# Kernel tuning notes

Measured on AMD Instinct MI355X. Metric: run time of the kernel, lower is better.

## Reference

```python
import jax, jax.numpy as jnp
import numpy as np

N = 100000      # nodes
E = 1250000     # edges
D = 64          # hidden_units == dim_node_features
DE = 7          # edge feature dim (OGBG-PPA)
L = 5           # num_layers
G = 128         # graphs in batch
T = 37          # classes


def setup_inputs() -> dict:
    key = jax.random.key(0)
    ks = jax.random.split(key, 12)
    x = jax.random.normal(ks[0], (N, D), dtype=jnp.float32)
    edge_index = jax.random.randint(ks[1], (2, E), 0, N, dtype=jnp.int64)
    edge_attr = jax.random.uniform(ks[2], (E, DE), dtype=jnp.float32)
    batch = jnp.sort(jax.random.randint(ks[3], (N,), 0, G, dtype=jnp.int64))
    s_e = 1.0 / np.sqrt(DE)
    s_d = 1.0 / np.sqrt(D)
    s_p = 1.0 / np.sqrt(L * D)
    W_edge = jax.random.normal(ks[4], (DE, D), dtype=jnp.float32) * s_e  # shared edge encoder
    b_edge = jnp.zeros((D,), jnp.float32)
    W_mlp = jax.random.normal(ks[5], (L, D, D), dtype=jnp.float32) * s_d  # per-layer MLP
    b_mlp = jnp.zeros((L, D), jnp.float32)
    eps = jnp.zeros((L,), jnp.float32)  # torch.Tensor([0]) per layer
    W_pred = jax.random.normal(ks[6], (L * D, T), dtype=jnp.float32) * s_p
    b_pred = jnp.zeros((T,), jnp.float32)
    return {"x": x, "edge_index": edge_index, "edge_attr": edge_attr, "batch": batch,
            "W_edge": W_edge, "b_edge": b_edge, "eps": eps,
            "W_mlp": W_mlp, "b_mlp": b_mlp, "W_pred": W_pred, "b_pred": b_pred}


def reference(x, edge_index, edge_attr, batch, W_edge, b_edge, eps, W_mlp, b_mlp, W_pred, b_pred):
    src, dst = edge_index[0], edge_index[1]  # PyG source_to_target: x_j = x[src], aggregate at dst
    # shared edge encoder -> identical output every layer; compute once
    edge_emb = edge_attr @ W_edge + b_edge  # [E, D]
    h = x
    outs = []
    for i in range(L):
        msg = jax.nn.relu(h[src] + edge_emb)                      # gather + fuse  [E, D]
        agg = jax.ops.segment_sum(msg, dst, num_segments=N)       # scatter-add    [N, D]
        h = jax.nn.relu(((1.0 + eps[i]) * h + agg) @ W_mlp[i] + b_mlp[i])
        outs.append(h)
    node_emb = jnp.concatenate(outs, axis=1)                      # [N, L*D]
    # predictor: per-graph mean pool + linear readout
    g_sum = jax.ops.segment_sum(node_emb, batch, num_segments=G)  # [G, L*D]
    cnt = jax.ops.segment_sum(jnp.ones((N, 1), node_emb.dtype), batch, num_segments=G)
    g = g_sum / jnp.maximum(cnt, 1.0)
    return g @ W_pred + b_pred                                    # [G, T]
```

## Files before the change

kernel.cpp:

```cpp
#include <hip/hip_runtime.h>
#include <hip/hip_bf16.h>

#define DD   64
#define NL   5
#define NT   37
#define LD   (NL*DD)
#define PB   16
#define NBMAX 512

typedef __attribute__((ext_vector_type(8))) short short8;
typedef __attribute__((ext_vector_type(4))) float f32x4;
typedef __attribute__((ext_vector_type(4))) int   i32x4;
typedef __attribute__((ext_vector_type(2))) int   i32x2;

static __device__ __forceinline__ int padq(int d) { return (d + PB - 1) & ~(PB - 1); }
static __device__ __forceinline__ short bf16_bits(float f) {
    __hip_bfloat16 h = __float2bfloat16(f);
    return __builtin_bit_cast(short, h);
}
static __device__ __forceinline__ float bf2f(short s) {
    return __int_as_float(((int)(unsigned short)s) << 16);
}

__global__ void init_kernel(const float* __restrict__ x, __hip_bfloat16* __restrict__ hb,
                            size_t n1, const float* __restrict__ W,
                            __hip_bfloat16* __restrict__ Wt, int n2,
                            const float* __restrict__ W_edge, const float* __restrict__ b_edge,
                            __hip_bfloat16* __restrict__ webt, int* __restrict__ bcnt,
                            const int* __restrict__ dst, int* __restrict__ deg, int E,
                            int do_deg) {
    size_t i = (size_t)blockIdx.x * blockDim.x + threadIdx.x;
    if (i < n1) {
        hb[i] = __float2bfloat16(x[i]);
    } else if (i < n1 + (size_t)n2) {
        size_t id = i - n1;
        int l = (int)(id / (DD * DD));
        int r = (int)(id % (DD * DD));
        int c = r / DD, k = r % DD;
        Wt[(size_t)l * DD * DD + c * DD + k] =
            __float2bfloat16(W[(size_t)l * DD * DD + k * DD + c]);
    } else if (i < n1 + (size_t)n2 + 2048) {
        int id = (int)(i - n1 - (size_t)n2);
        int f = id >> 5, k = id & 31;
        float v = (k < 7) ? W_edge[k * DD + f] : (k == 7 ? b_edge[f] : 0.f);
        webt[id] = __float2bfloat16(v);
    } else if (i < n1 + (size_t)n2 + 2048 + NBMAX) {
        bcnt[i - n1 - (size_t)n2 - 2048] = 0;
    } else if (do_deg) {
        size_t e = i - n1 - (size_t)n2 - 2048 - NBMAX;
        if (e < (size_t)E) atomicAdd(&deg[dst[e]], 1);
    }
}

__global__ void bhist_kernel(const int* __restrict__ dst, int* __restrict__ bcnt, int E) {
    __shared__ int h[NBMAX];
    int tid = threadIdx.x;
    h[tid] = 0; h[tid + 256] = 0;
    __syncthreads();
    int base = blockIdx.x * 4096;
#pragma unroll
    for (int j = 0; j < 16; ++j) {
        int e = base + j * 256 + tid;
        if (e < E) atomicAdd(&h[dst[e] >> 8], 1);
    }
    __syncthreads();
    int c0 = h[tid], c1 = h[tid + 256];
    if (c0) atomicAdd(&bcnt[tid], c0);
    if (c1) atomicAdd(&bcnt[tid + 256], c1);
}

__global__ void bscan_kernel(const int* __restrict__ bcnt, int* __restrict__ boff,
                             int* __restrict__ bcur) {
    __shared__ int sm[256];
    int tid = threadIdx.x;
    int v0 = bcnt[2 * tid], v1 = bcnt[2 * tid + 1];
    int s = v0 + v1;
    sm[tid] = s;
    __syncthreads();
    for (int off = 1; off < 256; off <<= 1) {
        int t = (tid >= off) ? sm[tid - off] : 0;
        __syncthreads();
        sm[tid] += t;
        __syncthreads();
    }
    int p = sm[tid] - s;
    boff[2 * tid] = p;     bcur[2 * tid] = p;     p += v0;
    boff[2 * tid + 1] = p; bcur[2 * tid + 1] = p; p += v1;
    if (tid == 255) boff[512] = p;
}

__global__ void pscat_kernel(const int* __restrict__ dst, int* __restrict__ bcur,
                             i32x2* __restrict__ stage, int E) {
    __shared__ int h[NBMAX];
    __shared__ int runb[NBMAX];
    int tid = threadIdx.x;
    h[tid] = 0; h[tid + 256] = 0;
    __syncthreads();
    int base = blockIdx.x * 4096;
    int d[16];
#pragma unroll
    for (int j = 0; j < 16; ++j) {
        int e = base + j * 256 + tid;
        d[j] = (e < E) ? dst[e] : -1;
        if (d[j] >= 0) atomicAdd(&h[d[j] >> 8], 1);
    }
    __syncthreads();
    int c0 = h[tid], c1 = h[tid + 256];
    runb[tid]       = c0 ? atomicAdd(&bcur[tid], c0) : 0;
    runb[tid + 256] = c1 ? atomicAdd(&bcur[tid + 256], c1) : 0;
    __syncthreads();
    h[tid] = 0; h[tid + 256] = 0;
    __syncthreads();
#pragma unroll
    for (int j = 0; j < 16; ++j) {
        if (d[j] >= 0) {
            int b = d[j] >> 8;
            int r = atomicAdd(&h[b], 1);
            i32x2 pr; pr[0] = base + j * 256 + tid; pr[1] = d[j];
            stage[runb[b] + r] = pr;
        }
    }
}

__global__ void bdeg_kernel(const i32x2* __restrict__ stage, const int* __restrict__ boff,
                            int* __restrict__ deg, int n) {
    __shared__ int cnt[256];
    int tid = threadIdx.x;
    int b = blockIdx.x;
    cnt[tid] = 0;
    __syncthreads();
    int s = boff[b], e = boff[b + 1];
    for (int j = s + tid; j < e; j += 256)
        atomicAdd(&cnt[stage[j][1] & 255], 1);
    __syncthreads();
    int node = b * 256 + tid;
    if (node < n) deg[node] = cnt[tid];
}

template<bool PACKED>
__global__ void assign_kernel(i32x2* __restrict__ stage, const int* __restrict__ boff,
                              const int* __restrict__ rowptr,
                              short* __restrict__ eab, int* __restrict__ srcv,
                              int* __restrict__ col, int n) {
    __shared__ int cur[256];
    int tid = threadIdx.x;
    int b = blockIdx.x;
    int node = b * 256 + tid;
    cur[tid] = (node < n) ? rowptr[node] : 0;
    __syncthreads();
    int s = boff[b], e = boff[b + 1];
    for (int j = s + tid; j < e; j += 256) {
        int d = stage[j][1];
        int slot = atomicAdd(&cur[d & 255], 1);
        stage[j][1] = slot;
    }
    __syncthreads();
    if (node < n) {
        int endp = rowptr[node + 1];
        for (int i = cur[tid]; i < endp; ++i) {
            srcv[i] = 0;
            if (PACKED) {
                i32x4 z = {0, 0, 0, 0};
                *((i32x4*)(eab + (size_t)i * 8)) = z;
            } else {
                col[i] = 0;
            }
        }
    }
}

template<bool PACKED>
__global__ void build_kernel(const i32x2* __restrict__ stage, const int* __restrict__ src,
                             const float* __restrict__ ea,
                             short* __restrict__ eab, int* __restrict__ srcv,
                             int* __restrict__ col, int E) {
    int j = blockIdx.x * blockDim.x + threadIdx.x;
    if (j >= E) return;
    i32x2 pr = stage[j];
    int eid = pr[0], slot = pr[1];
    srcv[slot] = src[eid];
    if (PACKED) {
        const float* a = ea + (size_t)eid * 7;
        short8 r;
#pragma unroll
        for (int k = 0; k < 7; ++k) r[k] = bf16_bits(a[k]);
        r[7] = (short)0x3F80;
        *((i32x4*)(eab + (size_t)slot * 8)) = __builtin_bit_cast(i32x4, r);
    } else {
        col[slot] = eid;
    }
}

__global__ void chunksum_kernel(const int* __restrict__ deg, int* __restrict__ csum, int n) {
    __shared__ int sm[256];
    int tid = threadIdx.x;
    int base = blockIdx.x * 1024 + tid * 4;
    int s = 0;
#pragma unroll
    for (int j = 0; j < 4; ++j) s += (base + j < n) ? padq(deg[base + j]) : 0;
    sm[tid] = s;
    __syncthreads();
    for (int off = 128; off > 0; off >>= 1) {
        if (tid < off) sm[tid] += sm[tid + off];
        __syncthreads();
    }
    if (tid == 0) csum[blockIdx.x] = sm[0];
}

__global__ void scansums_kernel(int* __restrict__ csum, int nc, int* __restrict__ tot) {
    __shared__ int sm[256];
    int tid = threadIdx.x;
    int base = tid * 4;
    int v[4]; int s = 0;
#pragma unroll
    for (int j = 0; j < 4; ++j) { v[j] = (base + j < nc) ? csum[base + j] : 0; s += v[j]; }
    sm[tid] = s;
    __syncthreads();
    for (int off = 1; off < 256; off <<= 1) {
        int t = (tid >= off) ? sm[tid - off] : 0;
        __syncthreads();
        sm[tid] += t;
        __syncthreads();
    }
    int p = sm[tid] - s;
#pragma unroll
    for (int j = 0; j < 4; ++j) { if (base + j < nc) csum[base + j] = p; p += v[j]; }
    if (tid == 255) *tot = p;
}

__global__ void chunkscan_kernel(const int* __restrict__ deg, const int* __restrict__ csum,
                                 int* __restrict__ rowptr, int* __restrict__ cursor, int n) {
    __shared__ int sm[256];
    int tid = threadIdx.x;
    int base = blockIdx.x * 1024 + tid * 4;
    int v[4]; int s = 0;
#pragma unroll
    for (int j = 0; j < 4; ++j) { v[j] = (base + j < n) ? padq(deg[base + j]) : 0; s += v[j]; }
    sm[tid] = s;
    __syncthreads();
    for (int off = 1; off < 256; off <<= 1) {
        int t = (tid >= off) ? sm[tid - off] : 0;
        __syncthreads();
        sm[tid] += t;
        __syncthreads();
    }
    int p = sm[tid] - s + csum[blockIdx.x];
#pragma unroll
    for (int j = 0; j < 4; ++j) {
        if (base + j < n) { rowptr[base + j] = p; cursor[base + j] = p; }
        p += v[j];
    }
}

__global__ void fillpos_kernel(const int* __restrict__ dst, int* __restrict__ cursor,
                               int* __restrict__ col, int E) {
    int e = blockIdx.x * blockDim.x + threadIdx.x;
    if (e >= E) return;
    int p = atomicAdd(&cursor[dst[e]], 1);
    col[p] = e;
}

__global__ void padmark_kernel(const int* __restrict__ deg, const int* __restrict__ rowptr,
                               int* __restrict__ col, int n) {
    int v = blockIdx.x * blockDim.x + threadIdx.x;
    if (v >= n) return;
    int s = rowptr[v] + deg[v];
    int e = rowptr[v + 1];
    for (int i = s; i < e; ++i) col[i] = -1;
}

template<bool PACKED>
__global__ void gfill_kernel(const int* __restrict__ col, const int* __restrict__ src,
                             const float* __restrict__ ea, const int* __restrict__ rowptrN,
                             short* __restrict__ eab, int* __restrict__ srcv,
                             int* __restrict__ colw) {
    int slot = blockIdx.x * blockDim.x + threadIdx.x;
    if (slot >= *rowptrN) return;
    int e = col[slot];
    int s = 0;
    short8 r;
#pragma unroll
    for (int k = 0; k < 8; ++k) r[k] = 0;
    if (e >= 0) {
        s = src[e];
        if (PACKED) {
            const float* a = ea + (size_t)e * 7;
#pragma unroll
            for (int k = 0; k < 7; ++k) r[k] = bf16_bits(a[k]);
            r[7] = (short)0x3F80;
        }
    } else if (!PACKED) {
        colw[slot] = 0;
    }
    __builtin_nontemporal_store(s, &srcv[slot]);
    if (PACKED) {
        i32x4 ri = __builtin_bit_cast(i32x4, r);
        __builtin_nontemporal_store(ri, (i32x4*)(eab + (size_t)slot * 8));
    }
}

template<bool PACKED>
__global__ void fill_kernel(const int* __restrict__ dst, const int* __restrict__ src,
                            const float* __restrict__ ea, int* __restrict__ cursor,
                            short* __restrict__ eab, int* __restrict__ col,
                            int* __restrict__ srcv, int E) {
    int e = blockIdx.x * blockDim.x + threadIdx.x;
    if (e >= E) return;
    int p = atomicAdd(&cursor[dst[e]], 1);
    int s = src[e];
    __builtin_nontemporal_store(s, &srcv[p]);
    if (PACKED) {
        const float* a = ea + (size_t)e * 7;
        short8 r;
#pragma unroll
        for (int k = 0; k < 7; ++k) r[k] = bf16_bits(a[k]);
        r[7] = (short)0x3F80;
        i32x4 ri = __builtin_bit_cast(i32x4, r);
        __builtin_nontemporal_store(ri, (i32x4*)(eab + (size_t)p * 8));
    } else {
        __builtin_nontemporal_store(e, &col[p]);
    }
}

__global__ void padfill_kernel(const int* __restrict__ deg, const int* __restrict__ rowptr,
                               int* __restrict__ srcv, int* __restrict__ col,
                               int has_col, int n) {
    int v = blockIdx.x * blockDim.x + threadIdx.x;
    if (v >= n) return;
    int s = rowptr[v] + deg[v];
    int e = rowptr[v + 1];
    for (int i = s; i < e; ++i) {
        srcv[i] = 0;
        if (has_col) col[i] = 0;
    }
}

template<bool PACKED>
static __device__ __forceinline__ float row_partial(
    const __hip_bfloat16* __restrict__ hb_in, const short* __restrict__ eab,
    const int* __restrict__ col, const float* __restrict__ ea,
    const int* __restrict__ srcv, int beg, int dv, int lane,
    const float* __restrict__ we, float be) {
    float acc = 0.f;
    int end = beg + dv;
    for (int p = beg; p < end; p += PB) {
        int mm = end - p;
        int S[PB];
#pragma unroll
        for (int j = 0; j < PB; ++j) S[j] = srcv[p + j];
        __hip_bfloat16 hv[PB];
#pragma unroll
        for (int j = 0; j < PB; ++j) hv[j] = hb_in[(size_t)S[j] * DD + lane];
        float ev[PB][7];
        if (PACKED) {
            short8 eb[PB];
#pragma unroll
            for (int j = 0; j < PB; ++j)
                eb[j] = *((const short8*)(eab + (size_t)(p + j) * 8));
#pragma unroll
            for (int j = 0; j < PB; ++j)
#pragma unroll
                for (int k = 0; k < 7; ++k) ev[j][k] = bf2f(eb[j][k]);
        } else {
            int EJ[PB];
#pragma unroll
            for (int j = 0; j < PB; ++j) EJ[j] = col[p + j];
#pragma unroll
            for (int j = 0; j < PB; ++j) {
                const float* a = ea + (size_t)EJ[j] * 7;
#pragma unroll
                for (int k = 0; k < 7; ++k) ev[j][k] = a[k];
            }
        }
#pragma unroll
        for (int j = 0; j < PB; ++j) {
            if (j < mm) {
                float emb = be + ev[j][0] * we[0] + ev[j][1] * we[1] + ev[j][2] * we[2]
                               + ev[j][3] * we[3] + ev[j][4] * we[4] + ev[j][5] * we[5]
                               + ev[j][6] * we[6];
                float tv = __bfloat162float(hv[j]) + emb;
                acc += (tv > 0.f) ? tv : 0.f;
            }
        }
    }
    return acc;
}

template<bool PACKED>
static __device__ __forceinline__ void agg_pair(
    const __hip_bfloat16* __restrict__ hb_in, const short* __restrict__ eab,
    const int* __restrict__ col, const float* __restrict__ ea,
    const int* __restrict__ srcv, int beg0, int d0, int beg1, int d1, bool has1,
    int lane, const float* __restrict__ we, float be, float& acc0, float& acc1) {
    acc0 = row_partial<PACKED>(hb_in, eab, col, ea, srcv, beg0, d0, lane, we, be);
    acc1 = 0.f;
    if (has1)
        acc1 = row_partial<PACKED>(hb_in, eab, col, ea, srcv, beg1, d1, lane, we, be);
}

__global__ __launch_bounds__(256, 4)
void aggmlp_kernel(const __hip_bfloat16* __restrict__ hb_in,
                   const short* __restrict__ eab, const int* __restrict__ srcv,
                   const int* __restrict__ rowptr, const int* __restrict__ deg,
                   const float* __restrict__ W_edge, const float* __restrict__ b_edge,
                   const __hip_bfloat16* __restrict__ webt,
                   const float* __restrict__ eps, int layer,
                   const __hip_bfloat16* __restrict__ Wt, const float* __restrict__ bmlp,
                   __hip_bfloat16* __restrict__ hb_out, int n) {
    __shared__ __align__(16) short uls[16][72];
    const unsigned short* hbu = (const unsigned short*)hb_in;
    int tid = threadIdx.x;
    int lane = tid & 63;
    int wv = __builtin_amdgcn_readfirstlane(tid >> 6);
    int base = blockIdx.x * 16;
    int colx = lane & 15;
    int q = lane >> 4;

    float we[7];
#pragma unroll
    for (int k = 0; k < 7; ++k) we[k] = W_edge[k * DD + lane];
    float be = b_edge[lane];
    float epsv = 1.f + eps[layer];

    short8 wb[4];
#pragma unroll
    for (int t = 0; t < 4; ++t)
        wb[t] = *((const short8*)(webt + (size_t)(t * 16 + colx) * 32 + q * 8));

#pragma unroll
    for (int nd = 0; nd < 4; ++nd) {
        int v = base + wv * 4 + nd;
        if (v < n) {
            int p = rowptr[v];
            int d = deg[v];
            float nodeacc;
            if (d >= 1 && d <= PB) {
                short8 a = {0, 0, 0, 0, 0, 0, 0, 0};
                if (q == 0)
                    a = *((const short8*)(eab + (size_t)(p + colx) * 8));
                int sr0 = srcv[p + 4 * q + 0];
                int sr1 = srcv[p + 4 * q + 1];
                int sr2 = srcv[p + 4 * q + 2];
                int sr3 = srcv[p + 4 * q + 3];
                f32x4 z = {0.f, 0.f, 0.f, 0.f};
                f32x4 emb[4];
#pragma unroll
                for (int t = 0; t < 4; ++t)
                    emb[t] = __builtin_amdgcn_mfma_f32_16x16x32_bf16(a, wb[t], z, 0, 0, 0);
                unsigned short hv[4][4];
#pragma unroll
                for (int t = 0; t < 4; ++t) {
                    hv[0][t] = hbu[(size_t)sr0 * DD + t * 16 + colx];
                    hv[1][t] = hbu[(size_t)sr1 * DD + t * 16 + colx];
                    hv[2][t] = hbu[(size_t)sr2 * DD + t * 16 + colx];
                    hv[3][t] = hbu[(size_t)sr3 * DD + t * 16 + colx];
                }
                float ts[4];
#pragma unroll
                for (int t = 0; t < 4; ++t) {
                    float s = 0.f;
#pragma unroll
                    for (int r = 0; r < 4; ++r) {
                        float tv = __int_as_float((int)hv[r][t] << 16) + emb[t][r];
                        float rv = ((4 * q + r) < d) ? ((tv > 0.f) ? tv : 0.f) : 0.f;
                        s += rv;
                    }
                    s += __shfl_xor(s, 16, 64);
                    s += __shfl_xor(s, 32, 64);
                    ts[t] = s;
                }
                nodeacc = (q == 0) ? ts[0] : (q == 1) ? ts[1] : (q == 2) ? ts[2] : ts[3];
            } else {
                nodeacc = row_partial<true>(hb_in, eab, nullptr, nullptr, srcv,
                                            p, d, lane, we, be);
            }
            float self = __int_as_float((int)hbu[(size_t)v * DD + lane] << 16);
            uls[wv * 4 + nd][lane] = bf16_bits(epsv * self + nodeacc);
        }
    }
    __syncthreads();

    if (wv == 0) {
        short8 wf[4][2];
#pragma unroll
        for (int t = 0; t < 4; ++t)
#pragma unroll
            for (int s = 0; s < 2; ++s)
                wf[t][s] = *((const short8*)(Wt + (size_t)(t * 16 + colx) * DD + s * 32 + q * 8));
        float bias[4];
#pragma unroll
        for (int t = 0; t < 4; ++t) bias[t] = bmlp[t * 16 + colx];

        short8 a0 = *((const short8*)&uls[colx][q * 8]);
        short8 a1 = *((const short8*)&uls[colx][32 + q * 8]);

        f32x4 acc[4] = {{0.f, 0.f, 0.f, 0.f}, {0.f, 0.f, 0.f, 0.f},
                        {0.f, 0.f, 0.f, 0.f}, {0.f, 0.f, 0.f, 0.f}};
#pragma unroll
        for (int t = 0; t < 4; ++t) {
            acc[t] = __builtin_amdgcn_mfma_f32_16x16x32_bf16(a0, wf[t][0], acc[t], 0, 0, 0);
            acc[t] = __builtin_amdgcn_mfma_f32_16x16x32_bf16(a1, wf[t][1], acc[t], 0, 0, 0);
        }
#pragma unroll
        for (int r = 0; r < 4; ++r) {
            int v = base + q * 4 + r;
            if (v < n) {
#pragma unroll
                for (int t = 0; t < 4; ++t) {
                    float val = acc[t][r] + bias[t];
                    val = (val > 0.f) ? val : 0.f;
                    hb_out[(size_t)v * DD + t * 16 + colx] = __float2bfloat16(val);
                }
            }
        }
    }
}

template<bool PACKED>
__global__ __launch_bounds__(256, 4)
void agg_kernel(const __hip_bfloat16* __restrict__ hb_in,
                const short* __restrict__ eab,
                const int* __restrict__ col, const int* __restrict__ srcv,
                const float* __restrict__ ea,
                const int* __restrict__ rowptr, const int* __restrict__ deg,
                const float* __restrict__ W_edge, const float* __restrict__ b_edge,
                const float* __restrict__ eps, int layer,
                __hip_bfloat16* __restrict__ u, int n) {
    int lane = threadIdx.x & 63;
    int wid = __builtin_amdgcn_readfirstlane(blockIdx.x * 4 + (threadIdx.x >> 6));
    int v0 = wid * 2;
    if (v0 >= n) return;

    float we[7];
#pragma unroll
    for (int k = 0; k < 7; ++k) we[k] = W_edge[k * DD + lane];
    float be = b_edge[lane];
    float epsv = 1.f + eps[layer];

    int beg0 = rowptr[v0];
    int d0   = deg[v0];
    bool has1 = (v0 + 1) < n;
    int beg1 = has1 ? rowptr[v0 + 1] : 0;
    int d1   = has1 ? deg[v0 + 1] : 0;

    float acc0, acc1;
    agg_pair<PACKED>(hb_in, eab, col, ea, srcv, beg0, d0, beg1, d1, has1,
                     lane, we, be, acc0, acc1);

    float self0 = __bfloat162float(hb_in[(size_t)v0 * DD + lane]);
    u[(size_t)v0 * DD + lane] = __float2bfloat16(epsv * self0 + acc0);
    if (has1) {
        float self1 = __bfloat162float(hb_in[(size_t)(v0 + 1) * DD + lane]);
        u[(size_t)(v0 + 1) * DD + lane] = __float2bfloat16(epsv * self1 + acc1);
    }
}

__global__ __launch_bounds__(256, 4)
void mlp_mfma_kernel(const __hip_bfloat16* __restrict__ u,
                     const __hip_bfloat16* __restrict__ Wt,
                     const float* __restrict__ bmlp,
                     __hip_bfloat16* __restrict__ hb_out, int n) {
    int lane = threadIdx.x & 63;
    int wid  = threadIdx.x >> 6;
    int colx = lane & 15;
    int quad = lane >> 4;
    int v0 = __builtin_amdgcn_readfirstlane((blockIdx.x * 4 + wid) * 16);
    if (v0 >= n) return;

    short8 wf[4][2];
#pragma unroll
    for (int t = 0; t < 4; ++t)
#pragma unroll
        for (int s = 0; s < 2; ++s)
            wf[t][s] = *((const short8*)(Wt + (size_t)(t * 16 + colx) * DD + s * 32 + quad * 8));
    float bias[4];
#pragma unroll
    for (int t = 0; t < 4; ++t) bias[t] = bmlp[t * 16 + colx];

    int vr = v0 + colx;
    int vrc = (vr < n) ? vr : (n - 1);
    const __hip_bfloat16* up = u + (size_t)vrc * DD;
    short8 a0 = *((const short8*)(up + quad * 8));
    short8 a1 = *((const short8*)(up + 32 + quad * 8));

    f32x4 acc[4] = {{0.f, 0.f, 0.f, 0.f}, {0.f, 0.f, 0.f, 0.f},
                    {0.f, 0.f, 0.f, 0.f}, {0.f, 0.f, 0.f, 0.f}};
#pragma unroll
    for (int t = 0; t < 4; ++t) {
        acc[t] = __builtin_amdgcn_mfma_f32_16x16x32_bf16(a0, wf[t][0], acc[t], 0, 0, 0);
        acc[t] = __builtin_amdgcn_mfma_f32_16x16x32_bf16(a1, wf[t][1], acc[t], 0, 0, 0);
    }

#pragma unroll
    for (int r = 0; r < 4; ++r) {
        int v = v0 + quad * 4 + r;
        if (v < n) {
#pragma unroll
            for (int t = 0; t < 4; ++t) {
                float val = acc[t][r] + bias[t];
                val = (val > 0.f) ? val : 0.f;
                hb_out[(size_t)v * DD + t * 16 + colx] = __float2bfloat16(val);
            }
        }
    }
}

__global__ void pool_part_kernel(const __hip_bfloat16* __restrict__ htabs, size_t lstride,
                                 const int* __restrict__ batch,
                                 float* __restrict__ g_sum, int n, int G) {
    __shared__ float part[4][DD];
    __shared__ int bnd[2];
    int g = blockIdx.x / NL;
    int q = blockIdx.x % NL;
    int tid = threadIdx.x;
    if (tid < 2) {
        int target = g + tid;
        int lo = 0, hi = n;
        while (lo < hi) { int mid = (lo + hi) >> 1; if (batch[mid] < target) lo = mid + 1; else hi = mid; }
        bnd[tid] = lo;
    }
    __syncthreads();
    int lb = bnd[0], ub = bnd[1];
    int w = tid >> 6, f = tid & 63;
    const __hip_bfloat16* T = htabs + (size_t)q * lstride;
    float s = 0.f;
    for (int v = lb + w; v < ub; v += 4)
        s += __bfloat162float(T[(size_t)v * DD + f]);
    part[w][f] = s;
    __syncthreads();
    if (tid < DD) {
        float tot = part[0][f] + part[1][f] + part[2][f] + part[3][f];
        float c = (float)(ub - lb);
        if (c < 1.f) c = 1.f;
        g_sum[(size_t)g * LD + q * DD + f] = tot / c;
    }
}

__global__ void readout_mean_kernel(const float* __restrict__ g_mean,
                                    const float* __restrict__ W_pred,
                                    const float* __restrict__ b_pred,
                                    float* __restrict__ out, int G) {
    int id = blockIdx.x * blockDim.x + threadIdx.x;
    if (id >= G * NT) return;
    int g = id / NT, t = id % NT;
    float acc = b_pred[t];
    const float* gs = g_mean + (size_t)g * LD;
    for (int k = 0; k < LD; ++k) acc += gs[k] * W_pred[k * NT + t];
    out[id] = acc;
}

__global__ void pool_kernel(const __hip_bfloat16* __restrict__ h, const int* __restrict__ batch,
                            float* __restrict__ g_sum, int layer, int n) {
    int wave = (blockIdx.x * blockDim.x + threadIdx.x) >> 6;
    int l = threadIdx.x & 63;
    int v0 = wave * 64;
    if (v0 >= n) return;
    int vend = min(v0 + 64, n);
    int cur = batch[v0];
    float acc = 0.f;
    for (int v = v0; v < vend; ++v) {
        int bv = batch[v];
        if (bv != cur) {
            atomicAdd(&g_sum[(size_t)cur * LD + layer * DD + l], acc);
            acc = 0.f;
            cur = bv;
        }
        acc += __bfloat162float(h[(size_t)v * DD + l]);
    }
    atomicAdd(&g_sum[(size_t)cur * LD + layer * DD + l], acc);
}

__global__ void graph_cnt_kernel(const int* __restrict__ batch, int* __restrict__ cnt,
                                 int n, int G) {
    int g = blockIdx.x * blockDim.x + threadIdx.x;
    if (g >= G) return;
    int lo = 0, hi = n;
    while (lo < hi) { int mid = (lo + hi) >> 1; if (batch[mid] < g) lo = mid + 1; else hi = mid; }
    int lb0 = lo;
    lo = lb0; hi = n;
    while (lo < hi) { int mid = (lo + hi) >> 1; if (batch[mid] < g + 1) lo = mid + 1; else hi = mid; }
    cnt[g] = lo - lb0;
}

__global__ void readout_kernel(const float* __restrict__ g_sum, const int* __restrict__ cnt,
                               const float* __restrict__ W_pred, const float* __restrict__ b_pred,
                               float* __restrict__ out, int G) {
    int id = blockIdx.x * blockDim.x + threadIdx.x;
    if (id >= G * NT) return;
    int g = id / NT, t = id % NT;
    float c = (float)cnt[g];
    if (c < 1.f) c = 1.f;
    float inv = 1.f / c;
    float acc = b_pred[t];
    const float* gs = g_sum + (size_t)g * LD;
    for (int k = 0; k < LD; ++k) acc += gs[k] * inv * W_pred[k * NT + t];
    out[id] = acc;
}

extern "C" void kernel_launch(void* const* d_in, const int* in_sizes, int n_in,
                              void* d_out, int out_size, void* d_ws, size_t ws_size,
                              hipStream_t stream) {
    const float* x       = (const float*)d_in[0];
    const int*   eidx    = (const int*)d_in[1];
    const float* ea      = (const float*)d_in[2];
    const int*   batch   = (const int*)d_in[3];
    const float* W_edge  = (const float*)d_in[4];
    const float* b_edge  = (const float*)d_in[5];
    const float* eps     = (const float*)d_in[6];
    const float* W_mlp   = (const float*)d_in[7];
    const float* b_mlp   = (const float*)d_in[8];
    const float* W_pred  = (const float*)d_in[9];
    const float* b_pred  = (const float*)d_in[10];
    float* out = (float*)d_out;

    const int N = in_sizes[3];
    const int E = in_sizes[2] / 7;
    const int G = out_size / NT;
    const int* src = eidx;
    const int* dst = eidx + E;
    const int NC = (N + 1023) / 1024;
    const int NB = (N + 255) >> 8;
    const size_t SLOTS = (size_t)E + (size_t)(PB - 1) * N;

    const size_t S_h = (size_t)N * DD * 2;
    const size_t small = (size_t)N * 4 + (size_t)(N + 4) * 4 + (size_t)N * 4 + 4096
                       + 8192 + 4096
                       + (size_t)NL * DD * DD * 2
                       + (size_t)G * LD * 4 + (((size_t)G * 4 + 15) & ~(size_t)15);
    const size_t needA = 7 * S_h + small + SLOTS * 20;
    const size_t needB = 7 * S_h + small + SLOTS * 8;
    const int tier = (ws_size >= needA) ? 0 : (ws_size >= needB) ? 1 : 2;
    const int nTab = (tier <= 1) ? 6 : 2;

    char* w = (char*)d_ws;
    __hip_bfloat16* hbt = (__hip_bfloat16*)w;  w += (size_t)nTab * S_h;
    __hip_bfloat16* u   = (__hip_bfloat16*)w;  w += S_h;
    __hip_bfloat16* Wt  = (__hip_bfloat16*)w;  w += (size_t)NL * DD * DD * 2;
    __hip_bfloat16* webt = (__hip_bfloat16*)w; w += 4096;
    int*   deg    = (int*)w;                   w += (size_t)N * 4;
    int*   rowptr = (int*)w;                   w += (size_t)(N + 4) * 4;
    int*   cursor = (int*)w;                   w += (size_t)N * 4;
    int*   csum   = (int*)w;                   w += 4096;
    int*   bcnt   = (int*)w;                   w += 2048;
    int*   boff   = (int*)w;                   w += 2064;
    int*   bcur   = (int*)w;                   w += 2048;
    float* g_sum  = (float*)w;                 w += (size_t)G * LD * 4;
    int*   cnt    = (int*)w;                   w += ((size_t)G * 4 + 15) & ~(size_t)15;
    short* eab = nullptr; int* col = nullptr; int* srcv = nullptr;
    if (tier == 0) {
        eab  = (short*)w;  w += SLOTS * 16;
        srcv = (int*)w;
    } else {
        col  = (int*)w;    w += SLOTS * 4;
        srcv = (int*)w;
    }
    const bool packed = (tier == 0);

    const bool newcsr = (NB <= NBMAX) && ((size_t)E * 8 <= S_h);
    i32x2* stage = (i32x2*)u;

    if (tier == 2) hipMemsetAsync(g_sum, 0, (size_t)G * LD * 4, stream);

    {
        size_t n1 = (size_t)N * DD;
        size_t tot = n1 + (size_t)(NL * DD * DD) + 2048 + NBMAX + (newcsr ? 0 : (size_t)E);
        if (!newcsr) hipMemsetAsync(deg, 0, (size_t)N * 4, stream);
        init_kernel<<<(unsigned)((tot + 255) / 256), 256, 0, stream>>>(
            x, hbt, n1, W_mlp, Wt, NL * DD * DD, W_edge, b_edge, webt, bcnt,
            dst, deg, E, newcsr ? 0 : 1);
    }

    if (newcsr) {
        unsigned eb4 = (unsigned)((E + 4095) / 4096);
        bhist_kernel<<<eb4, 256, 0, stream>>>(dst, bcnt, E);
        bscan_kernel<<<1, 256, 0, stream>>>(bcnt, boff, bcur);
        pscat_kernel<<<eb4, 256, 0, stream>>>(dst, bcur, stage, E);
        bdeg_kernel<<<NB, 256, 0, stream>>>(stage, boff, deg, N);
        chunksum_kernel<<<NC, 256, 0, stream>>>(deg, csum, N);
        scansums_kernel<<<1, 256, 0, stream>>>(csum, NC, rowptr + N);
        chunkscan_kernel<<<NC, 256, 0, stream>>>(deg, csum, rowptr, cursor, N);
        if (packed) {
            assign_kernel<true><<<NB, 256, 0, stream>>>(stage, boff, rowptr,
                                                        eab, srcv, col, N);
            build_kernel<true><<<(E + 255) / 256, 256, 0, stream>>>(stage, src, ea,
                                                                    eab, srcv, col, E);
        } else {
            assign_kernel<false><<<NB, 256, 0, stream>>>(stage, boff, rowptr,
                                                         eab, srcv, col, N);
            build_kernel<false><<<(E + 255) / 256, 256, 0, stream>>>(stage, src, ea,
                                                                     eab, srcv, col, E);
        }
    } else {
        chunksum_kernel<<<NC, 256, 0, stream>>>(deg, csum, N);
        scansums_kernel<<<1, 256, 0, stream>>>(csum, NC, rowptr + N);
        chunkscan_kernel<<<NC, 256, 0, stream>>>(deg, csum, rowptr, cursor, N);
        int* colbuf = nullptr;
        if (tier == 0) {
            if (SLOTS * 4 <= S_h) colbuf = (int*)u;
        } else {
            colbuf = col;
        }
        if (colbuf) {
            fillpos_kernel<<<(E + 255) / 256, 256, 0, stream>>>(dst, cursor, colbuf, E);
            padmark_kernel<<<(N + 255) / 256, 256, 0, stream>>>(deg, rowptr, colbuf, N);
            unsigned gblocks = (unsigned)((SLOTS + 255) / 256);
            if (packed)
                gfill_kernel<true><<<gblocks, 256, 0, stream>>>(colbuf, src, ea, rowptr + N,
                                                                eab, srcv, colbuf);
            else
                gfill_kernel<false><<<gblocks, 256, 0, stream>>>(colbuf, src, ea, rowptr + N,
                                                                 eab, srcv, colbuf);
        } else {
            if (packed)
                fill_kernel<true><<<(E + 255) / 256, 256, 0, stream>>>(dst, src, ea, cursor,
                                                                       eab, col, srcv, E);
            else
                fill_kernel<false><<<(E + 255) / 256, 256, 0, stream>>>(dst, src, ea, cursor,
                                                                        eab, col, srcv, E);
            padfill_kernel<<<(N + 255) / 256, 256, 0, stream>>>(deg, rowptr, srcv,
                                                                col ? col : srcv,
                                                                col ? 1 : 0, N);
        }
    }

    const bool useFused = newcsr && packed;
    int fusedBlocks = (N + 15) / 16;
    int aggBlocks = (N + 7) / 8;
    int mlpBlocks = (N + 63) / 64;
    for (int i = 0; i < NL; ++i) {
        __hip_bfloat16* hin  = (tier <= 1) ? (hbt + (size_t)i * N * DD)
                                           : (hbt + (size_t)(i & 1) * N * DD);
        __hip_bfloat16* hout = (tier <= 1) ? (hbt + (size_t)(i + 1) * N * DD)
                                           : (hbt + (size_t)((i + 1) & 1) * N * DD);
        if (useFused) {
            aggmlp_kernel<<<fusedBlocks, 256, 0, stream>>>(
                hin, eab, srcv, rowptr, deg, W_edge, b_edge, webt, eps, i,
                Wt + (size_t)i * DD * DD, b_mlp + (size_t)i * DD, hout, N);
        } else {
            if (packed)
                agg_kernel<true><<<aggBlocks, 256, 0, stream>>>(
                    hin, eab, col, srcv, ea, rowptr, deg, W_edge, b_edge, eps, i, u, N);
            else
                agg_kernel<false><<<aggBlocks, 256, 0, stream>>>(
                    hin, eab, col, srcv, ea, rowptr, deg, W_edge, b_edge, eps, i, u, N);
            mlp_mfma_kernel<<<mlpBlocks, 256, 0, stream>>>(
                u, Wt + (size_t)i * DD * DD, b_mlp + (size_t)i * DD, hout, N);
        }
        if (tier == 2)
            pool_kernel<<<((N + 63) / 64 * 64 + 255) / 256, 256, 0, stream>>>(hout, batch,
                                                                              g_sum, i, N);
    }

    if (tier <= 1) {
        pool_part_kernel<<<G * NL, 256, 0, stream>>>(hbt + (size_t)N * DD, (size_t)N * DD,
                                                     batch, g_sum, N, G);
        readout_mean_kernel<<<(G * NT + 255) / 256, 256, 0, stream>>>(g_sum, W_pred, b_pred,
                                                                      out, G);
    } else {
        graph_cnt_kernel<<<1, 128, 0, stream>>>(batch, cnt, N, G);
        readout_kernel<<<(G * NT + 255) / 256, 256, 0, stream>>>(g_sum, cnt, W_pred, b_pred,
                                                                 out, G);
    }
}
```

Before: 615.6 us.

## Bucket-scatter full edge records then gather into CSR via inverse slot map

Adds a packed-tier CSR build path. The partition-scatter kernel now writes the source index and bf16-packed edge attributes into bucket-ordered staging buffers, which reuse spare hidden-state memory. An assign kernel then records, for each CSR slot, which staged edge belongs there. A final move kernel gathers from staging and writes the CSR arrays with coalesced nontemporal stores. This replaces the old build kernel's random scattered writes of 16-byte records and its random reads of src and edge_attr by edge id, at the cost of one extra kernel and an extra staging pass.

```diff
diff --git a/kernel.cpp b/kernel.cpp
--- a/kernel.cpp
+++ b/kernel.cpp
@@ -122,6 +122,48 @@
     }
 }
 
+__global__ void pscat2_kernel(const int* __restrict__ dst, const int* __restrict__ src,
+                              const float* __restrict__ ea, int* __restrict__ bcur,
+                              i32x2* __restrict__ meta, i32x4* __restrict__ rec, int E) {
+    __shared__ int h[NBMAX];
+    __shared__ int runb[NBMAX];
+    int tid = threadIdx.x;
+    h[tid] = 0; h[tid + 256] = 0;
+    __syncthreads();
+    int base = blockIdx.x * 4096;
+    int d[16];
+#pragma unroll
+    for (int j = 0; j < 16; ++j) {
+        int e = base + j * 256 + tid;
+        d[j] = (e < E) ? dst[e] : -1;
+        if (d[j] >= 0) atomicAdd(&h[d[j] >> 8], 1);
+    }
+    __syncthreads();
+    int c0 = h[tid], c1 = h[tid + 256];
+    runb[tid]       = c0 ? atomicAdd(&bcur[tid], c0) : 0;
+    runb[tid + 256] = c1 ? atomicAdd(&bcur[tid + 256], c1) : 0;
+    __syncthreads();
+    h[tid] = 0; h[tid + 256] = 0;
+    __syncthreads();
+#pragma unroll
+    for (int j = 0; j < 16; ++j) {
+        if (d[j] >= 0) {
+            int e = base + j * 256 + tid;
+            int b = d[j] >> 8;
+            int r = atomicAdd(&h[b], 1);
+            int pos = runb[b] + r;
+            i32x2 m; m[0] = src[e]; m[1] = d[j];
+            meta[pos] = m;
+            const float* a = ea + (size_t)e * 7;
+            short8 rr;
+#pragma unroll
+            for (int k = 0; k < 7; ++k) rr[k] = bf16_bits(a[k]);
+            rr[7] = (short)0x3F80;
+            rec[pos] = __builtin_bit_cast(i32x4, rr);
+        }
+    }
+}
+
 __global__ void bdeg_kernel(const i32x2* __restrict__ stage, const int* __restrict__ boff,
                             int* __restrict__ deg, int n) {
     __shared__ int cnt[256];
@@ -167,6 +209,43 @@
             }
         }
     }
+}
+
+__global__ void assign2_kernel(const i32x2* __restrict__ meta, const int* __restrict__ boff,
+                               const int* __restrict__ rowptr, int* __restrict__ inv, int n) {
+    __shared__ int cur[256];
+    int tid = threadIdx.x;
+    int b = blockIdx.x;
+    int node = b * 256 + tid;
+    cur[tid] = (node < n) ? rowptr[node] : 0;
+    __syncthreads();
+    int s = boff[b], e = boff[b + 1];
+    for (int j = s + tid; j < e; j += 256) {
+        int d = meta[j][1];
+        int slot = atomicAdd(&cur[d & 255], 1);
+        inv[slot] = j;
+    }
+    __syncthreads();
+    if (node < n) {
+        int endp = rowptr[node + 1];
+        for (int i = cur[tid]; i < endp; ++i) inv[i] = -1;
+    }
+}
+
+__global__ void move2_kernel(const int* __restrict__ inv, const i32x2* __restrict__ meta,
+                             const i32x4* __restrict__ rec, const int* __restrict__ rowptrN,
+                             short* __restrict__ eab, int* __restrict__ srcv) {
+    int slot = blockIdx.x * blockDim.x + threadIdx.x;
+    if (slot >= *rowptrN) return;
+    int pos = inv[slot];
+    int s = 0;
+    i32x4 r = {0, 0, 0, 0};
+    if (pos >= 0) {
+        s = meta[pos][0];
+        r = rec[pos];
+    }
+    __builtin_nontemporal_store(s, &srcv[slot]);
+    __builtin_nontemporal_store(r, (i32x4*)(eab + (size_t)slot * 8));
 }
 
 template<bool PACKED>
@@ -757,7 +836,12 @@
     const bool packed = (tier == 0);
 
     const bool newcsr = (NB <= NBMAX) && ((size_t)E * 8 <= S_h);
+    const bool newpk = newcsr && packed &&
+                       ((size_t)E * 16 <= 2 * S_h) && (SLOTS * 4 <= S_h);
     i32x2* stage = (i32x2*)u;
+    i32x2* meta  = (i32x2*)(hbt + (size_t)1 * N * DD);
+    i32x4* rec   = (i32x4*)(hbt + (size_t)2 * N * DD);
+    int*   inv   = (int*)u;
 
     if (tier == 2) hipMemsetAsync(g_sum, 0, (size_t)G * LD * 4, stream);
 
@@ -774,21 +858,33 @@
         unsigned eb4 = (unsigned)((E + 4095) / 4096);
         bhist_kernel<<<eb4, 256, 0, stream>>>(dst, bcnt, E);
         bscan_kernel<<<1, 256, 0, stream>>>(bcnt, boff, bcur);
-        pscat_kernel<<<eb4, 256, 0, stream>>>(dst, bcur, stage, E);
-        bdeg_kernel<<<NB, 256, 0, stream>>>(stage, boff, deg, N);
-        chunksum_kernel<<<NC, 256, 0, stream>>>(deg, csum, N);
-        scansums_kernel<<<1, 256, 0, stream>>>(csum, NC, rowptr + N);
-        chunkscan_kernel<<<NC, 256, 0, stream>>>(deg, csum, rowptr, cursor, N);
-        if (packed) {
-            assign_kernel<true><<<NB, 256, 0, stream>>>(stage, boff, rowptr,
-                                                        eab, srcv, col, N);
-            build_kernel<true><<<(E + 255) / 256, 256, 0, stream>>>(stage, src, ea,
-                                                                    eab, srcv, col, E);
+        if (newpk) {
+            pscat2_kernel<<<eb4, 256, 0, stream>>>(dst, src, ea, bcur, meta, rec, E);
+            bdeg_kernel<<<NB, 256, 0, stream>>>(meta, boff, deg, N);
+            chunksum_kernel<<<NC, 256, 0, stream>>>(deg, csum, N);
+            scansums_kernel<<<1, 256, 0, stream>>>(csum, NC, rowptr + N);
+            chunkscan_kernel<<<NC, 256, 0, stream>>>(deg, csum, rowptr, cursor, N);
+            assign2_kernel<<<NB, 256, 0, stream>>>(meta, boff, rowptr, inv, N);
+            unsigned mblocks = (unsigned)((SLOTS + 255) / 256);
+            move2_kernel<<<mblocks, 256, 0, stream>>>(inv, meta, rec, rowptr + N,
+                                                      eab, srcv);
         } else {
-            assign_kernel<false><<<NB, 256, 0, stream>>>(stage, boff, rowptr,
-                                                         eab, srcv, col, N);
-            build_kernel<false><<<(E + 255) / 256, 256, 0, stream>>>(stage, src, ea,
-                                                                     eab, srcv, col, E);
+            pscat_kernel<<<eb4, 256, 0, stream>>>(dst, bcur, stage, E);
+            bdeg_kernel<<<NB, 256, 0, stream>>>(stage, boff, deg, N);
+            chunksum_kernel<<<NC, 256, 0, stream>>>(deg, csum, N);
+            scansums_kernel<<<1, 256, 0, stream>>>(csum, NC, rowptr + N);
+            chunkscan_kernel<<<NC, 256, 0, stream>>>(deg, csum, rowptr, cursor, N);
+            if (packed) {
+                assign_kernel<true><<<NB, 256, 0, stream>>>(stage, boff, rowptr,
+                                                            eab, srcv, col, N);
+                build_kernel<true><<<(E + 255) / 256, 256, 0, stream>>>(stage, src, ea,
+                                                                        eab, srcv, col, E);
+            } else {
+                assign_kernel<false><<<NB, 256, 0, stream>>>(stage, boff, rowptr,
+                                                             eab, srcv, col, N);
+                build_kernel<false><<<(E + 255) / 256, 256, 0, stream>>>(stage, src, ea,
+                                                                         eab, srcv, col, E);
+            }
         }
     } else {
         chunksum_kernel<<<NC, 256, 0, stream>>>(deg, csum, N);
```

Measured after the change: 632.6 us. 2.8% more time.
